# Performance work log

Measured on AMD Instinct MI355X. Metric: run time of the kernel, lower is better.

The kernel has to match this reference:

```python
import jax, jax.numpy as jnp
import numpy as np

N = 100000      # nodes
IN = 256        # in_feats
H = 256         # h_feats
C = 2           # num_classes
E = 400000      # edges per relation
DST_MAX = [70000, 80000, 75000]  # dst ranges -> guarantees isolated nodes per relation


def _build_rel(rng, dst_max):
    """Build one relation: edges, degree mask, induced subgraph on non-isolated nodes."""
    src = rng.integers(0, N, size=E)
    dst = rng.integers(0, dst_max, size=E)
    deg = np.bincount(dst, minlength=N)
    keep = np.where(deg > 0)[0].astype(np.int32)   # nodes with in_degree > 0 (original order)
    iso = np.where(deg == 0)[0].astype(np.int32)   # isolated nodes (original order)
    inv = np.full(N, -1, dtype=np.int64)
    inv[keep] = np.arange(len(keep))
    m = inv[src] >= 0                              # DGL node subgraph keeps edges with both endpoints in set
    ssrc = inv[src[m]].astype(np.int32)
    sdst = inv[dst[m]].astype(np.int32)
    sdeg = np.bincount(sdst, minlength=len(keep))
    norm = (1.0 / np.sqrt(np.clip(sdeg, 1, None))).astype(np.float32)  # D^{-1/2}, clamp(min=1)
    return keep, iso, ssrc, sdst, norm


def setup_inputs() -> dict:
    rng = np.random.default_rng(0)
    key = jax.random.key(0)
    ks = jax.random.split(key, 20)
    d = {"in_feat": jax.random.normal(ks[0], (N, IN), jnp.float32)}
    for r, dm in enumerate(DST_MAX):
        keep, iso, ssrc, sdst, norm = _build_rel(rng, dm)
        d[f"keep{r}"] = jnp.asarray(keep)
        d[f"iso{r}"] = jnp.asarray(iso)
        d[f"src{r}"] = jnp.asarray(ssrc)
        d[f"dst{r}"] = jnp.asarray(sdst)
        d[f"norm{r}"] = jnp.asarray(norm)
        d[f"lam{r}"] = jnp.float32(1.99)  # stand-in for dgl.laplacian_lambda_max (~2 for large graphs)
    s = 0.02
    def W(k, i, o):
        return s * jax.random.normal(k, (i, o), jnp.float32)
    d["W_lin"] = W(ks[1], IN, H);   d["b_lin"] = jnp.zeros((H,), jnp.float32)
    d["W2"]    = W(ks[2], H, H);    d["b2"]    = jnp.zeros((H,), jnp.float32)
    d["W1sg"]  = W(ks[3], H, H);    d["b1sg"]  = jnp.zeros((H,), jnp.float32)
    d["W2sg"]  = W(ks[4], H, H);    d["b2sg"]  = jnp.zeros((H,), jnp.float32)
    d["Wc1"]   = W(ks[5], 2 * H, H); d["bc1"]  = jnp.zeros((H,), jnp.float32)  # ChebConv k=2: Linear(k*H, H)
    d["Wc2"]   = W(ks[6], 2 * H, H); d["bc2"]  = jnp.zeros((H,), jnp.float32)
    d["W3"]    = W(ks[7], 2 * H, H); d["b3"]   = jnp.zeros((H,), jnp.float32)
    d["W4"]    = W(ks[8], H, C);    d["b4"]    = jnp.zeros((C,), jnp.float32)
    return d


def _cheb(x, src, dst, norm, lam, Wc, bc):
    """DGL ChebConv, k=2: X0=x; X1=-re*(D^-.5 A D^-.5 x)+(re-1)*x; relu(Linear([X0,X1]))."""
    re = 2.0 / lam
    xn = x * norm[:, None]
    agg = jax.ops.segment_sum(xn[src], dst, num_segments=x.shape[0]) * norm[:, None]
    X1 = -re * agg + x * (re - 1.0)
    return jax.nn.relu(jnp.concatenate([x, X1], axis=-1) @ Wc + bc)


def reference(in_feat,
              keep0, iso0, src0, dst0, norm0, lam0,
              keep1, iso1, src1, dst1, norm1, lam1,
              keep2, iso2, src2, dst2, norm2, lam2,
              W_lin, b_lin, W2, b2, W1sg, b1sg, W2sg, b2sg,
              Wc1, bc1, Wc2, bc2, W3, b3, W4, b4):
    def block(h, keep, iso, src, dst, norm, lam):
        hk = h[keep]                                   # non-isolated nodes
        h01 = _cheb(hk, src, dst, norm, lam, Wc1, bc1)
        h11 = _cheb(h01, src, dst, norm, lam, Wc2, bc2)
        h02 = h[iso] @ W1sg + b1sg                     # isolated-node branch
        h12 = h02 @ W2sg + b2sg
        h_final = jnp.concatenate([
            jnp.concatenate([h01, h11], axis=-1),      # [M, 2H]
            jnp.concatenate([h02, h12], axis=-1),      # [N-M, 2H]
        ], axis=0)                                     # note: permuted node order, as in original
        return h_final @ W3 + b3

    h = jax.nn.leaky_relu(in_feat @ W_lin + b_lin)
    h = jax.nn.leaky_relu(h @ W2 + b2)
    h_all = []
    rels = [(keep0, iso0, src0, dst0, norm0, lam0),
            (keep1, iso1, src1, dst1, norm1, lam1),
            (keep2, iso2, src2, dst2, norm2, lam2)]
    for rel in rels:
        h = block(h, *rel)   # h is re-used across relations, faithfully to the torch code
        h_all.append(h)
    out = jax.nn.leaky_relu(h_all[0] + h_all[1] + h_all[2])
    return out @ W4 + b4
```

## Files before the change

kernel.cpp:

```cpp
#include <hip/hip_runtime.h>
#include <cstddef>

typedef unsigned short bf16;
typedef short bf16x8 __attribute__((ext_vector_type(8)));
typedef float f32x4 __attribute__((ext_vector_type(4)));
#define LREL 0.01f

__device__ __forceinline__ float bf2f(unsigned int u) {
    union { unsigned int i; float f; } c; c.i = u << 16; return c.f;
}
__device__ __forceinline__ bf16 f2bf(float f) {
    union { unsigned int i; float f; } c; c.f = f;
    return (bf16)((c.i + 0x7FFFu + ((c.i >> 16) & 1u)) >> 16);
}
__device__ __forceinline__ unsigned int pack2(float a, float b) {
    return (unsigned int)f2bf(a) | ((unsigned int)f2bf(b) << 16);
}
__device__ __forceinline__ float activate(float v, int ACT) {
    if (ACT == 1) return v > 0.f ? v : 0.f;
    if (ACT == 2) return v > 0.f ? v : LREL * v;
    return v;
}

template<int ACT, bool DUAL, int ACCMODE, bool GATHER, bool AFP32>
__global__ __launch_bounds__(256) void gemm_mfma(
    const void* __restrict__ A1v, const int* __restrict__ rows1,
    const bf16* __restrict__ A2,
    const bf16* __restrict__ WT1, const bf16* __restrict__ WT2,
    const float* __restrict__ bias,
    bf16* __restrict__ C, bf16* __restrict__ Cacc, int M)
{
    __shared__ bf16 As[128 * 64];
    __shared__ bf16 Bs[128 * 64];
    const int tid  = threadIdx.x;
    const int lane = tid & 63;
    const int wv   = tid >> 6;
    const int wr   = wv >> 1, wc = wv & 1;
    const int row0 = blockIdx.x * 128;
    const int col0 = blockIdx.y * 128;

    f32x4 acc[4][4];
#pragma unroll
    for (int mi = 0; mi < 4; ++mi)
#pragma unroll
        for (int ni = 0; ni < 4; ++ni)
#pragma unroll
            for (int e = 0; e < 4; ++e) acc[mi][ni][e] = 0.f;

    const int ar = tid & 127;
    const int kh = tid >> 7;
    const int arow = min(row0 + ar, M - 1);
    const size_t aoff1 = (size_t)(GATHER ? rows1[arow] : arow) * 256;
    const size_t aoff2 = (size_t)arow * 256;
    const int bn = ar;

    const int nparts = DUAL ? 2 : 1;
    for (int part = 0; part < nparts; ++part) {
        const bf16* __restrict__ WT = (part == 0) ? WT1 : WT2;
        for (int kt = 0; kt < 256; kt += 64) {
            uint4 areg[4], breg[4];
#pragma unroll
            for (int cc = 0; cc < 4; ++cc) {
                const int c = kh * 4 + cc;
                if (part == 0) {
                    if constexpr (AFP32) {
                        const float* p = (const float*)A1v + aoff1 + kt + c * 8;
                        float4 f0 = *(const float4*)p;
                        float4 f1 = *(const float4*)(p + 4);
                        areg[cc].x = pack2(f0.x, f0.y); areg[cc].y = pack2(f0.z, f0.w);
                        areg[cc].z = pack2(f1.x, f1.y); areg[cc].w = pack2(f1.z, f1.w);
                    } else {
                        areg[cc] = *(const uint4*)((const bf16*)A1v + aoff1 + kt + c * 8);
                    }
                } else {
                    areg[cc] = *(const uint4*)(A2 + aoff2 + kt + c * 8);
                }
                breg[cc] = *(const uint4*)(WT + (size_t)(col0 + bn) * 256 + kt + c * 8);
            }
            __syncthreads();
#pragma unroll
            for (int cc = 0; cc < 4; ++cc) {
                const int c = kh * 4 + cc;
                *(uint4*)(As + ar * 64 + 8 * (c ^ (ar & 7))) = areg[cc];
                *(uint4*)(Bs + bn * 64 + 8 * (c ^ (bn & 7))) = breg[cc];
            }
            __syncthreads();
#pragma unroll
            for (int ks = 0; ks < 2; ++ks) {
                bf16x8 af[4], bfr[4];
#pragma unroll
                for (int mi = 0; mi < 4; ++mi) {
                    const int r = wr * 64 + mi * 16 + (lane & 15);
                    const int c = ks * 4 + (lane >> 4);
                    af[mi] = *(const bf16x8*)(As + r * 64 + 8 * (c ^ (r & 7)));
                }
#pragma unroll
                for (int ni = 0; ni < 4; ++ni) {
                    const int n = wc * 64 + ni * 16 + (lane & 15);
                    const int c = ks * 4 + (lane >> 4);
                    bfr[ni] = *(const bf16x8*)(Bs + n * 64 + 8 * (c ^ (n & 7)));
                }
#pragma unroll
                for (int mi = 0; mi < 4; ++mi)
#pragma unroll
                    for (int ni = 0; ni < 4; ++ni)
                        acc[mi][ni] = __builtin_amdgcn_mfma_f32_16x16x32_bf16(
                            af[mi], bfr[ni], acc[mi][ni], 0, 0, 0);
            }
        }
    }

#pragma unroll
    for (int mi = 0; mi < 4; ++mi) {
#pragma unroll
        for (int reg = 0; reg < 4; ++reg) {
            const int r = row0 + wr * 64 + mi * 16 + (lane >> 4) * 4 + reg;
            if (r < M) {
#pragma unroll
                for (int ni = 0; ni < 4; ++ni) {
                    const int cx = col0 + wc * 64 + ni * 16 + (lane & 15);
                    float v = activate(acc[mi][ni][reg] + bias[cx], ACT);
                    C[(size_t)r * 256 + cx] = f2bf(v);
                    if constexpr (ACCMODE == 1) {
                        Cacc[(size_t)r * 256 + cx] = f2bf(v);
                    } else if constexpr (ACCMODE == 2) {
                        float o = bf2f(Cacc[(size_t)r * 256 + cx]);
                        Cacc[(size_t)r * 256 + cx] = f2bf(o + v);
                    }
                }
            }
        }
    }
}

__global__ void wconv_all(const float* __restrict__ W_lin, const float* __restrict__ W2,
                          const float* __restrict__ W1sg, const float* __restrict__ W2sg,
                          const float* __restrict__ Wc1, const float* __restrict__ Wc2,
                          const float* __restrict__ W3, bf16* __restrict__ out)
{
    const int b = blockIdx.x;
    const int m = b >> 8, k = b & 255, n = threadIdx.x;
    const float* src;
    switch (m) {
        case 0: src = W_lin; break;       case 1: src = W2; break;
        case 2: src = W1sg; break;        case 3: src = W2sg; break;
        case 4: src = Wc1; break;         case 5: src = Wc1 + 65536; break;
        case 6: src = Wc2; break;         case 7: src = Wc2 + 65536; break;
        case 8: src = W3; break;          default: src = W3 + 65536; break;
    }
    out[(size_t)m * 65536 + n * 256 + k] = f2bf(src[k * 256 + n]);
}

template<bool GATHER>
__global__ void agg_x1(const bf16* __restrict__ x, const int* __restrict__ gidx,
                       const float* __restrict__ norm,
                       const int* __restrict__ rp, const int* __restrict__ ssrc,
                       const float* __restrict__ lam, bf16* __restrict__ X1, int M)
{
    int d = blockIdx.x * 4 + (threadIdx.x >> 6);
    if (d >= M) return;
    int l = threadIdx.x & 63;
    float s0 = 0.f, s1 = 0.f, s2 = 0.f, s3 = 0.f;
    int e0 = rp[d], e1 = rp[d + 1];
    for (int e = e0; e < e1; ++e) {
        int si = ssrc[e];
        float nv = norm[si];
        const bf16* xr = x + (size_t)(GATHER ? gidx[si] : si) * 256 + l * 4;
        uint2 u = *(const uint2*)xr;
        s0 += bf2f(u.x & 0xFFFFu) * nv; s1 += bf2f(u.x >> 16) * nv;
        s2 += bf2f(u.y & 0xFFFFu) * nv; s3 += bf2f(u.y >> 16) * nv;
    }
    float re = 2.0f / lam[0];
    float a = -re * norm[d];
    float b = re - 1.0f;
    const bf16* xdp = x + (size_t)(GATHER ? gidx[d] : d) * 256 + l * 4;
    uint2 xd = *(const uint2*)xdp;
    uint2 o;
    o.x = pack2(a * s0 + b * bf2f(xd.x & 0xFFFFu), a * s1 + b * bf2f(xd.x >> 16));
    o.y = pack2(a * s2 + b * bf2f(xd.y & 0xFFFFu), a * s3 + b * bf2f(xd.y >> 16));
    *(uint2*)(X1 + (size_t)d * 256 + l * 4) = o;
}

__global__ void zero_k(int* __restrict__ p, int n)
{
    int i = blockIdx.x * 256 + threadIdx.x;
    if (i < n) p[i] = 0;
}

__global__ void hist_k(const int* __restrict__ dst, int* __restrict__ deg, int E)
{
    int e = blockIdx.x * 256 + threadIdx.x;
    if (e < E) atomicAdd(&deg[dst[e]], 1);
}

__global__ void scan1_k(const int* __restrict__ deg, int* __restrict__ bsum, int M)
{
    __shared__ int red[256];
    int b = blockIdx.x, t = threadIdx.x;
    int base = b * 1024 + t * 4;
    int s = 0;
#pragma unroll
    for (int j = 0; j < 4; ++j) { int i = base + j; if (i < M) s += deg[i]; }
    red[t] = s; __syncthreads();
    for (int off = 128; off; off >>= 1) {
        if (t < off) red[t] += red[t + off];
        __syncthreads();
    }
    if (t == 0) bsum[b] = red[0];
}
__global__ void scan2_k(int* __restrict__ bsum, int nb, int* __restrict__ rp, int M)
{
    __shared__ int buf[256];
    int t = threadIdx.x;
    int v = (t < nb) ? bsum[t] : 0;
    buf[t] = v; __syncthreads();
    for (int off = 1; off < 256; off <<= 1) {
        int y = (t >= off) ? buf[t - off] : 0;
        __syncthreads();
        buf[t] += y;
        __syncthreads();
    }
    if (t < nb) bsum[t] = buf[t] - v;
    if (t == 0) rp[M] = buf[255];
}
__global__ void scan3_k(const int* __restrict__ deg, const int* __restrict__ bsum,
                        int* __restrict__ rp, int M)
{
    __shared__ int buf[256];
    int b = blockIdx.x, t = threadIdx.x;
    int base = b * 1024 + t * 4;
    int v0 = (base + 0 < M) ? deg[base + 0] : 0;
    int v1 = (base + 1 < M) ? deg[base + 1] : 0;
    int v2 = (base + 2 < M) ? deg[base + 2] : 0;
    int v3 = (base + 3 < M) ? deg[base + 3] : 0;
    int s = v0 + v1 + v2 + v3;
    buf[t] = s; __syncthreads();
    for (int off = 1; off < 256; off <<= 1) {
        int y = (t >= off) ? buf[t - off] : 0;
        __syncthreads();
        buf[t] += y;
        __syncthreads();
    }
    int ex = bsum[b] + buf[t] - s;
    if (base + 0 < M) rp[base + 0] = ex;
    if (base + 1 < M) rp[base + 1] = ex + v0;
    if (base + 2 < M) rp[base + 2] = ex + v0 + v1;
    if (base + 3 < M) rp[base + 3] = ex + v0 + v1 + v2;
}

__global__ void scatter_k(const int* __restrict__ src, const int* __restrict__ dst,
                          const int* __restrict__ rp, int* __restrict__ cursor,
                          int* __restrict__ out, int E)
{
    int e = blockIdx.x * 256 + threadIdx.x;
    if (e < E) {
        int d = dst[e];
        int pos = rp[d] + atomicAdd(&cursor[d], 1);
        out[pos] = src[e];
    }
}

__global__ void final_k(const bf16* __restrict__ acc, const float* __restrict__ W4,
                        const float* __restrict__ b4, float* __restrict__ out, int Nn)
{
    int r = blockIdx.x * 4 + (threadIdx.x >> 6);
    if (r >= Nn) return;
    int l = threadIdx.x & 63;
    uint2 u = *(const uint2*)(acc + (size_t)r * 256 + l * 4);
    float v[4] = { bf2f(u.x & 0xFFFFu), bf2f(u.x >> 16),
                   bf2f(u.y & 0xFFFFu), bf2f(u.y >> 16) };
    float s0 = 0.f, s1 = 0.f;
#pragma unroll
    for (int j = 0; j < 4; ++j) {
        float x = v[j] > 0.f ? v[j] : LREL * v[j];
        int k = l * 4 + j;
        s0 += x * W4[k * 2 + 0];
        s1 += x * W4[k * 2 + 1];
    }
#pragma unroll
    for (int off = 32; off; off >>= 1) {
        s0 += __shfl_xor(s0, off, 64);
        s1 += __shfl_xor(s1, off, 64);
    }
    if (l == 0) {
        out[(size_t)r * 2 + 0] = s0 + b4[0];
        out[(size_t)r * 2 + 1] = s1 + b4[1];
    }
}

extern "C" void kernel_launch(void* const* d_in, const int* in_sizes, int n_in,
                              void* d_out, int out_size, void* d_ws, size_t ws_size,
                              hipStream_t stream)
{
    const float* in_feat = (const float*)d_in[0];
    const int Nn = in_sizes[0] / 256;

    const float* W_lin = (const float*)d_in[19]; const float* b_lin = (const float*)d_in[20];
    const float* W2p   = (const float*)d_in[21]; const float* b2   = (const float*)d_in[22];
    const float* W1sg  = (const float*)d_in[23]; const float* b1sg = (const float*)d_in[24];
    const float* W2sg  = (const float*)d_in[25]; const float* b2sg = (const float*)d_in[26];
    const float* Wc1   = (const float*)d_in[27]; const float* bc1  = (const float*)d_in[28];
    const float* Wc2   = (const float*)d_in[29]; const float* bc2  = (const float*)d_in[30];
    const float* W3p   = (const float*)d_in[31]; const float* b3   = (const float*)d_in[32];
    const float* W4p   = (const float*)d_in[33]; const float* b4   = (const float*)d_in[34];

    int Mr[3], NIr[3], Er[3];
    int M_max = 0, NI_max = 0, E_max = 0;
    for (int r = 0; r < 3; ++r) {
        Mr[r]  = in_sizes[1 + 6 * r];
        NIr[r] = in_sizes[2 + 6 * r];
        Er[r]  = in_sizes[3 + 6 * r];
        if (Mr[r] > M_max)  M_max  = Mr[r];
        if (NIr[r] > NI_max) NI_max = NIr[r];
        if (Er[r] > E_max)  E_max  = Er[r];
    }

    bf16* ACC = (bf16*)d_ws;
    bf16* H   = ACC + (size_t)Nn * 256;
    bf16* S1  = H + (size_t)Nn * 256;
    bf16* S2  = S1 + (size_t)M_max * 256;
    bf16* S3  = S2 + (size_t)M_max * 256;
    bf16* S4  = S3 + (size_t)M_max * 256;
    bf16* WTb = S4 + (size_t)NI_max * 256;
    int* deg    = (int*)(WTb + 10 * 65536);
    int* cursor = deg + (Nn + 1);
    int* rp     = cursor + (Nn + 1);
    int* bsum   = rp + (Nn + 1);
    int* ssrc   = bsum + 256;

    bf16* WT_lin = WTb;             bf16* WT_2   = WTb + 1 * 65536;
    bf16* WT_1sg = WTb + 2 * 65536; bf16* WT_2sg = WTb + 3 * 65536;
    bf16* WT_c1a = WTb + 4 * 65536; bf16* WT_c1b = WTb + 5 * 65536;
    bf16* WT_c2a = WTb + 6 * 65536; bf16* WT_c2b = WTb + 7 * 65536;
    bf16* WT_3a  = WTb + 8 * 65536; bf16* WT_3b  = WTb + 9 * 65536;

    auto g2 = [](int M) { return dim3((unsigned)((M + 127) / 128), 2); };

    wconv_all<<<2560, 256, 0, stream>>>(W_lin, W2p, W1sg, W2sg, Wc1, Wc2, W3p, WTb);

    gemm_mfma<2, false, 0, false, true><<<g2(Nn), 256, 0, stream>>>(
        in_feat, nullptr, nullptr, WT_lin, nullptr, b_lin, ACC, nullptr, Nn);
    gemm_mfma<2, false, 0, false, false><<<g2(Nn), 256, 0, stream>>>(
        ACC, nullptr, nullptr, WT_2, nullptr, b2, H, nullptr, Nn);

    for (int r = 0; r < 3; ++r) {
        const int*   keep = (const int*)d_in[1 + 6 * r];
        const int*   iso  = (const int*)d_in[2 + 6 * r];
        const int*   srcA = (const int*)d_in[3 + 6 * r];
        const int*   dstA = (const int*)d_in[4 + 6 * r];
        const float* norm = (const float*)d_in[5 + 6 * r];
        const float* lam  = (const float*)d_in[6 + 6 * r];
        const int M  = Mr[r];
        const int NI = NIr[r];
        const int E  = Er[r];
        const int nb = (M + 1023) / 1024;

        zero_k<<<(2 * (Nn + 1) + 255) / 256, 256, 0, stream>>>(deg, 2 * (Nn + 1));
        hist_k<<<(E + 255) / 256, 256, 0, stream>>>(dstA, deg, E);
        scan1_k<<<nb, 256, 0, stream>>>(deg, bsum, M);
        scan2_k<<<1, 256, 0, stream>>>(bsum, nb, rp, M);
        scan3_k<<<nb, 256, 0, stream>>>(deg, bsum, rp, M);
        scatter_k<<<(E + 255) / 256, 256, 0, stream>>>(srcA, dstA, rp, cursor, ssrc, E);

        agg_x1<true><<<(M + 3) / 4, 256, 0, stream>>>(H, keep, norm, rp, ssrc, lam, S1, M);
        gemm_mfma<1, true, 0, true, false><<<g2(M), 256, 0, stream>>>(
            H, keep, S1, WT_c1a, WT_c1b, bc1, S2, nullptr, M);
        agg_x1<false><<<(M + 3) / 4, 256, 0, stream>>>(S2, nullptr, norm, rp, ssrc, lam, S1, M);
        gemm_mfma<1, true, 0, false, false><<<g2(M), 256, 0, stream>>>(
            S2, nullptr, S1, WT_c2a, WT_c2b, bc2, S3, nullptr, M);

        gemm_mfma<0, false, 0, true, false><<<g2(NI), 256, 0, stream>>>(
            H, iso, nullptr, WT_1sg, nullptr, b1sg, S1, nullptr, NI);
        gemm_mfma<0, false, 0, false, false><<<g2(NI), 256, 0, stream>>>(
            S1, nullptr, nullptr, WT_2sg, nullptr, b2sg, S4, nullptr, NI);

        if (r == 0) {
            gemm_mfma<0, true, 1, false, false><<<g2(NI), 256, 0, stream>>>(
                S1, nullptr, S4, WT_3a, WT_3b, b3,
                H + (size_t)M * 256, ACC + (size_t)M * 256, NI);
            gemm_mfma<0, true, 1, false, false><<<g2(M), 256, 0, stream>>>(
                S2, nullptr, S3, WT_3a, WT_3b, b3, H, ACC, M);
        } else {
            gemm_mfma<0, true, 2, false, false><<<g2(NI), 256, 0, stream>>>(
                S1, nullptr, S4, WT_3a, WT_3b, b3,
                H + (size_t)M * 256, ACC + (size_t)M * 256, NI);
            gemm_mfma<0, true, 2, false, false><<<g2(M), 256, 0, stream>>>(
                S2, nullptr, S3, WT_3a, WT_3b, b3, H, ACC, M);
        }
    }

    final_k<<<(Nn + 3) / 4, 256, 0, stream>>>(ACC, W4p, b4, (float*)d_out, Nn);
}
```

Measured before the change: 2.619 ms.

## Swap MFMA operands for vectorized epilogue stores and reorder grid dims

New measurement: 2.576 ms. No clear change (-1.6%).

```diff
diff --git a/kernel.cpp b/kernel.cpp
--- a/kernel.cpp
+++ b/kernel.cpp
@@ -36,8 +36,8 @@
     const int lane = tid & 63;
     const int wv   = tid >> 6;
     const int wr   = wv >> 1, wc = wv & 1;
-    const int row0 = blockIdx.x * 128;
-    const int col0 = blockIdx.y * 128;
+    const int row0 = blockIdx.y * 128;
+    const int col0 = blockIdx.x * 128;
 
     f32x4 acc[4][4];
 #pragma unroll
@@ -105,28 +105,32 @@
 #pragma unroll
                     for (int ni = 0; ni < 4; ++ni)
                         acc[mi][ni] = __builtin_amdgcn_mfma_f32_16x16x32_bf16(
-                            af[mi], bfr[ni], acc[mi][ni], 0, 0, 0);
+                            bfr[ni], af[mi], acc[mi][ni], 0, 0, 0);
             }
         }
     }
 
 #pragma unroll
     for (int mi = 0; mi < 4; ++mi) {
-#pragma unroll
-        for (int reg = 0; reg < 4; ++reg) {
-            const int r = row0 + wr * 64 + mi * 16 + (lane >> 4) * 4 + reg;
-            if (r < M) {
-#pragma unroll
-                for (int ni = 0; ni < 4; ++ni) {
-                    const int cx = col0 + wc * 64 + ni * 16 + (lane & 15);
-                    float v = activate(acc[mi][ni][reg] + bias[cx], ACT);
-                    C[(size_t)r * 256 + cx] = f2bf(v);
-                    if constexpr (ACCMODE == 1) {
-                        Cacc[(size_t)r * 256 + cx] = f2bf(v);
-                    } else if constexpr (ACCMODE == 2) {
-                        float o = bf2f(Cacc[(size_t)r * 256 + cx]);
-                        Cacc[(size_t)r * 256 + cx] = f2bf(o + v);
-                    }
+        const int r = row0 + wr * 64 + mi * 16 + (lane & 15);
+        if (r < M) {
+#pragma unroll
+            for (int ni = 0; ni < 4; ++ni) {
+                const int c0 = col0 + wc * 64 + ni * 16 + (lane >> 4) * 4;
+                float o[4];
+#pragma unroll
+                for (int reg = 0; reg < 4; ++reg)
+                    o[reg] = activate(acc[mi][ni][reg] + bias[c0 + reg], ACT);
+                uint2 cv; cv.x = pack2(o[0], o[1]); cv.y = pack2(o[2], o[3]);
+                *(uint2*)(C + (size_t)r * 256 + c0) = cv;
+                if constexpr (ACCMODE == 1) {
+                    *(uint2*)(Cacc + (size_t)r * 256 + c0) = cv;
+                } else if constexpr (ACCMODE == 2) {
+                    uint2 ov = *(const uint2*)(Cacc + (size_t)r * 256 + c0);
+                    uint2 nv2;
+                    nv2.x = pack2(bf2f(ov.x & 0xFFFFu) + o[0], bf2f(ov.x >> 16) + o[1]);
+                    nv2.y = pack2(bf2f(ov.y & 0xFFFFu) + o[2], bf2f(ov.y >> 16) + o[3]);
+                    *(uint2*)(Cacc + (size_t)r * 256 + c0) = nv2;
                 }
             }
         }
@@ -334,7 +338,7 @@
     bf16* WT_c2a = WTb + 6 * 65536; bf16* WT_c2b = WTb + 7 * 65536;
     bf16* WT_3a  = WTb + 8 * 65536; bf16* WT_3b  = WTb + 9 * 65536;
 
-    auto g2 = [](int M) { return dim3((unsigned)((M + 127) / 128), 2); };
+    auto g2 = [](int M) { return dim3(2u, (unsigned)((M + 127) / 128)); };
 
     wconv_all<<<2560, 256, 0, stream>>>(W_lin, W2p, W1sg, W2sg, Wc1, Wc2, W3p, WTb);
 
```
